# Performance work log

Measured on AMD Instinct MI355X. Metric: run time of the kernel, lower is better.

Reference implementation:

```python
import jax, jax.numpy as jnp
import numpy as np

B, N, D = 32, 2048, 1024


def setup_inputs() -> dict:
    key = jax.random.key(0)
    k1, k2, k3, k4, k5, k6 = jax.random.split(key, 6)
    encoded = jax.random.normal(k1, (B, N, D), dtype=jnp.float32)
    decoder_state = jax.random.normal(k2, (B, D), dtype=jnp.float32)
    mask = jax.random.randint(k3, (B, N), 0, 2, dtype=jnp.int32)
    scale = 1.0 / np.sqrt(D)
    W1 = jax.random.normal(k4, (D, D), dtype=jnp.float32) * scale  # applied as x @ W1
    W2 = jax.random.normal(k5, (D, D), dtype=jnp.float32) * scale
    vt = jax.random.normal(k6, (D,), dtype=jnp.float32) * scale
    return {"encoded": encoded, "decoder_state": decoder_state, "mask": mask,
            "W1": W1, "W2": W2, "vt": vt}


def reference(encoded, decoder_state, mask, W1, W2, vt):
    temperature = 1.0
    # process_encoded: W1(encoded)  [B, N, D]
    enc = jnp.einsum('bnd,de->bne', encoded, W1)
    # W2(decoder_state)  [B, D] -> broadcast-add over N
    dec = decoder_state @ W2
    # vt(tanh(.)).squeeze(2)  -> logits [B, N]
    u = jnp.einsum('bnd,d->bn', jnp.tanh(enc + dec[:, None, :]), vt)
    # masked log-softmax with temperature over dim=1
    logits = u / temperature + jnp.log(mask.astype(u.dtype) + 1e-45)
    return jax.nn.log_softmax(logits, axis=1)
```

## Files before the change

### kernel.cpp

```cpp
#include <hip/hip_runtime.h>

typedef _Float16 half8 __attribute__((ext_vector_type(8)));
typedef _Float16 half4 __attribute__((ext_vector_type(4)));
typedef __fp16   pk2   __attribute__((ext_vector_type(2)));
typedef float    f32x4 __attribute__((ext_vector_type(4)));

#define GLOBAL_AS __attribute__((address_space(1)))
#define LDS_AS    __attribute__((address_space(3)))

static constexpr int Bb = 32;
static constexpr int Nn = 2048;
static constexpr int Dd = 1024;
static constexpr int M  = Bb * Nn;


__global__ void prep0(const float* __restrict__ W1, _Float16* __restrict__ W1TT,
                      const float* __restrict__ ds, const float* __restrict__ W2,
                      float* __restrict__ dec) {
    const int id = blockIdx.x;
    const int tid = threadIdx.x;
    if (id < 512) {
        int g = id * 256 + tid;
        int chunk = g >> 10;
        int u = g & 1023;
        int q = u >> 7, sc = u & 127;
        int cl = sc ^ (2 * (q & 3));
        int et = chunk >> 5, t = (chunk >> 1) & 15, h = chunk & 1;
        int e  = et * 256 + h * 128 + cl;
        int k0 = t * 64 + q * 8;
        half8 hh;
#pragma unroll
        for (int j = 0; j < 8; ++j)
            hh[j] = (_Float16)W1[(size_t)(k0 + j) * Dd + e];
        *(half8*)(W1TT + (size_t)g * 8) = hh;
    } else {
        __shared__ float part[4][64];
        const int id2 = id - 512;
        const int b = id2 >> 4, ech = id2 & 15;
        int e = ech * 64 + (tid & 63);
        int dc = tid >> 6;
        float acc = 0.f;
#pragma unroll 4
        for (int d = dc * 256; d < dc * 256 + 256; ++d)
            acc += ds[b * Dd + d] * W2[(size_t)d * Dd + e];
        part[dc][tid & 63] = acc;
        __syncthreads();
        if (tid < 64)
            dec[b * Dd + e] = part[0][tid] + part[1][tid]
                            + part[2][tid] + part[3][tid];
    }
}

#define BAR     asm volatile("s_barrier" ::: "memory")
#define LGKM(n) asm volatile("s_waitcnt lgkmcnt(" #n ")" ::: "memory")
#define VM(n)   asm volatile("s_waitcnt vmcnt(" #n ")" ::: "memory")
#define PRIO1   __builtin_amdgcn_s_setprio(1)
#define PRIO0   __builtin_amdgcn_s_setprio(0)

#define RD_A(dst, base) do { _Pragma("unroll") \
  for (int ks = 0; ks < 2; ++ks) { \
    _Pragma("unroll") for (int m2 = 0; m2 < 4; ++m2) { \
      const int row_ = m2 * 32 + rA; \
      const int kc0_ = (ks * 4 + qq) * 2; \
      dst[m2][ks] = *(const half8*)&lds[(base) + (row_ * 16 + (kc0_ ^ rxa)) * 4]; \
    } } } while (0)

#define RD_B(dst, base) do { _Pragma("unroll") \
  for (int ks = 0; ks < 2; ++ks) { const int qb = ((ks * 4 + qq) * 128) * 8; \
    _Pragma("unroll") for (int j2 = 0; j2 < 2; ++j2) \
      dst[j2][ks] = *(const half8*)&lds[(base) + qb + (j2 * 64 + rB) * 8]; } } while (0)

#define MFMAQ(A_, B_, ro, co) do { \
  _Pragma("unroll") for (int m2 = 0; m2 < 4; ++m2) \
  _Pragma("unroll") for (int j2 = 0; j2 < 2; ++j2) { \
    acc[(ro) + m2][(co) + j2] = __builtin_amdgcn_mfma_f32_16x16x32_f16( \
        A_[m2][0], B_[j2][0], acc[(ro) + m2][(co) + j2], 0, 0, 0); \
    acc[(ro) + m2][(co) + j2] = __builtin_amdgcn_mfma_f32_16x16x32_f16( \
        A_[m2][1], B_[j2][1], acc[(ro) + m2][(co) + j2], 0, 0, 0); } } while (0)

__global__ __launch_bounds__(512, 2) void gemm8(
    const float* __restrict__ encA, const _Float16* __restrict__ W1TT,
    const float* __restrict__ dec, const float* __restrict__ vt,
    float* __restrict__ u_part)
{
    extern __shared__ _Float16 lds[];

    const int g  = blockIdx.x;
    const int wg = (g & 7) * 128 + (g >> 3);
    const int et    = wg & 3;
    const int mtile = wg >> 2;

    const int tid  = threadIdx.x;
    const int lane = tid & 63, wid = tid >> 6;
    const int wr = wid >> 2, wc = wid & 3;
    const int qq = lane >> 4, l15 = lane & 15;
    const int l15s = l15 ^ (2 * qq);
    const int rA = wr * 16 + l15;
    const int rxa = (l15 & 7) * 2;
    const int rB = wc * 16 + l15s;

    f32x4 acc[8][4] = {};
    half8 a[4][2], b0[2][2], b1[2][2];
    f32x4 aSt[8];

    const int arow0 = tid >> 4;
    const int l16   = tid & 15;
    const float* agp = encA + (((size_t)(mtile * 256 + arow0)) << 10) + l16 * 4;

    const size_t bbase = (size_t)et * 32 * 8192;
    const int uoff = tid * 8;

    auto issueA = [&](int T) {
        const float* gp = agp + T * 64;
#pragma unroll
        for (int p = 0; p < 8; ++p)
            aSt[p] = *(const f32x4*)(gp + ((size_t)p << 15));
    };
    auto writeA = [&](int Tn) {
        const int base = (Tn & 1) << 14;
#pragma unroll
        for (int p = 0; p < 8; ++p) {
            const int rf = p * 32 + arow0;
            const int h  = rf >> 7, row = rf & 127;
            pk2 c0 = __builtin_amdgcn_cvt_pkrtz(aSt[p][0], aSt[p][1]);
            pk2 c1 = __builtin_amdgcn_cvt_pkrtz(aSt[p][2], aSt[p][3]);
            half4 hh; hh[0] = c0[0]; hh[1] = c0[1]; hh[2] = c1[0]; hh[3] = c1[1];
            *(half4*)&lds[base + h * 8192
                          + (row * 16 + (l16 ^ ((row & 7) * 2))) * 4] = hh;
        }
    };
    auto stB = [&](int T, int h) {
        const _Float16* gp = W1TT + bbase + ((size_t)(T * 2 + h) << 13) + uoff;
        _Float16* lp = lds + (32768 + (((T & 1) * 2 + h) << 13) + (wid << 9));
        __builtin_amdgcn_global_load_lds((const GLOBAL_AS void*)gp,
                                         (LDS_AS void*)lp, 16, 0, 0);
        __builtin_amdgcn_global_load_lds((const GLOBAL_AS void*)(gp + 4096),
                                         (LDS_AS void*)(lp + 4096), 16, 0, 0);
    };


    issueA(0); stB(0, 0); stB(0, 1);
    VM(4);
    writeA(0);
    VM(0); LGKM(0);
    BAR;

#pragma unroll 2
    for (int T = 0; T < 16; ++T) {
        const int As  = (T & 1) << 14;
        const int Bs2 = 32768 + ((T & 1) << 14);
        const bool s = (T < 15);

        if (s) { issueA(T + 1); stB(T + 1, 0); stB(T + 1, 1); }

        RD_A(a, As);
        RD_B(b0, Bs2);
        RD_B(b1, Bs2 + 8192);
        LGKM(4);
        PRIO1; MFMAQ(a, b0, 0, 0); PRIO0;
        LGKM(0);
        PRIO1; MFMAQ(a, b1, 0, 2); PRIO0;
        RD_A(a, As + 8192);
        LGKM(0);
        PRIO1; MFMAQ(a, b0, 4, 0); MFMAQ(a, b1, 4, 2); PRIO0;

        if (s) { VM(4); writeA(T + 1); }
        VM(0); LGKM(0);
        BAR;
    }

    const int b = mtile >> 3;
    float vtv[4], dcv[4];
#pragma unroll
    for (int nf = 0; nf < 4; ++nf) {
        int e = et * 256 + (nf >> 1) * 128 + (nf & 1) * 64 + wc * 16 + l15;
        vtv[nf] = vt[e];
        dcv[nf] = dec[b * Dd + e];
    }
    float* usum = (float*)lds;
#pragma unroll
    for (int hm = 0; hm < 8; ++hm) {
        const int h = hm >> 2, mq = hm & 3;
#pragma unroll
        for (int r = 0; r < 4; ++r) {
            float sv = 0.f;
#pragma unroll
            for (int nf = 0; nf < 4; ++nf) {
                float x  = acc[hm][nf][r] + dcv[nf];
                float ex = __expf(2.f * x);
                sv += (1.f - 2.f * __builtin_amdgcn_rcpf(ex + 1.f)) * vtv[nf];
            }
#pragma unroll
            for (int off = 1; off < 16; off <<= 1) sv += __shfl_xor(sv, off, 16);
            if (l15 == 0)
                usum[wc * 256 + h * 128 + mq * 32 + wr * 16 + qq * 4 + r] = sv;
        }
    }
    __syncthreads();
    if (tid < 256) {
        float v = usum[tid] + usum[256 + tid] + usum[512 + tid] + usum[768 + tid];
        u_part[(size_t)et * M + (size_t)mtile * 256 + tid] = v;
    }
}

__global__ void softmax_k(const float* __restrict__ up, const int* __restrict__ mask,
                          float* __restrict__ out) {
    __shared__ float red[8];
    int b = blockIdx.x, tid = threadIdx.x;
    float l[8];
#pragma unroll
    for (int i = 0; i < 8; ++i) {
        int n = i * 256 + tid;
        float s = up[(size_t)b * Nn + n];
#pragma unroll
        for (int et = 1; et < 4; ++et) s += up[(size_t)et * M + (size_t)b * Nn + n];
        l[i] = s + (mask[b * Nn + n] ? 0.f : -103.278931f);
    }
    float m = l[0];
#pragma unroll
    for (int i = 1; i < 8; ++i) m = fmaxf(m, l[i]);
#pragma unroll
    for (int o = 32; o >= 1; o >>= 1) m = fmaxf(m, __shfl_xor(m, o, 64));
    if ((tid & 63) == 0) red[tid >> 6] = m;
    __syncthreads();
    m = fmaxf(fmaxf(red[0], red[1]), fmaxf(red[2], red[3]));
    float s = 0.f;
#pragma unroll
    for (int i = 0; i < 8; ++i) s += expf(l[i] - m);
#pragma unroll
    for (int o = 32; o >= 1; o >>= 1) s += __shfl_xor(s, o, 64);
    if ((tid & 63) == 0) red[4 + (tid >> 6)] = s;
    __syncthreads();
    float lse = m + logf(red[4] + red[5] + red[6] + red[7]);
#pragma unroll
    for (int i = 0; i < 8; ++i)
        out[(size_t)b * Nn + i * 256 + tid] = l[i] - lse;
}

extern "C" void kernel_launch(void* const* d_in, const int* in_sizes, int n_in,
                              void* d_out, int out_size, void* d_ws, size_t ws_size,
                              hipStream_t stream) {
    const float* encoded = (const float*)d_in[0];
    const float* dstate  = (const float*)d_in[1];
    const int*   mask    = (const int*)d_in[2];
    const float* W1      = (const float*)d_in[3];
    const float* W2      = (const float*)d_in[4];
    const float* vt      = (const float*)d_in[5];
    float* out = (float*)d_out;

    char* ws = (char*)d_ws;
    float*    u_part = (float*)ws;
    float*    dec    = (float*)(ws + (size_t)4 * M * 4);
    _Float16* W1TT   = (_Float16*)(ws + (size_t)4 * M * 4 + (size_t)Bb * Dd * 4);

    static bool attr_done = false;
    if (!attr_done) {
        hipFuncSetAttribute(reinterpret_cast<const void*>(gemm8),
                            hipFuncAttributeMaxDynamicSharedMemorySize, 131072);
        attr_done = true;
    }

    prep0<<<1024, 256, 0, stream>>>(W1, W1TT, dstate, W2, dec);
    gemm8<<<1024, 512, 131072, stream>>>(encoded, W1TT, dec, vt, u_part);
    softmax_k<<<32, 256, 0, stream>>>(u_part, mask, out);
}
```

Baseline: 525.1 us.

## Make each workgroup loop over all E-tiles for one M-tile

The grid shrinks from 1024 to 256 workgroups, and each one now walks all four output-column tiles for its row tile in one 64-step loop. The tanh/vt epilogue runs every 16 steps and the accumulators are reset. The aim is for the four re-reads of the same encoded rows to hit cache, and to avoid launch and tail overhead. In exchange it gives one workgroup per CU with less latency hiding, and needs extra LDS for the reduction buffer.

```diff
diff --git a/kernel.cpp b/kernel.cpp
--- a/kernel.cpp
+++ b/kernel.cpp
@@ -86,9 +86,7 @@
     extern __shared__ _Float16 lds[];
 
     const int g  = blockIdx.x;
-    const int wg = (g & 7) * 128 + (g >> 3);
-    const int et    = wg & 3;
-    const int mtile = wg >> 2;
+    const int mtile = (g & 7) * 32 + (g >> 3);
 
     const int tid  = threadIdx.x;
     const int lane = tid & 63, wid = tid >> 6;
@@ -107,11 +105,11 @@
     const int l16   = tid & 15;
     const float* agp = encA + (((size_t)(mtile * 256 + arow0)) << 10) + l16 * 4;
 
-    const size_t bbase = (size_t)et * 32 * 8192;
     const int uoff = tid * 8;
-
-    auto issueA = [&](int T) {
-        const float* gp = agp + T * 64;
+    float* usum = (float*)(lds + 65536);
+
+    auto issueA = [&](int Tn) {
+        const float* gp = agp + (Tn & 15) * 64;
 #pragma unroll
         for (int p = 0; p < 8; ++p)
             aSt[p] = *(const f32x4*)(gp + ((size_t)p << 15));
@@ -129,9 +127,9 @@
                           + (row * 16 + (l16 ^ ((row & 7) * 2))) * 4] = hh;
         }
     };
-    auto stB = [&](int T, int h) {
-        const _Float16* gp = W1TT + bbase + ((size_t)(T * 2 + h) << 13) + uoff;
-        _Float16* lp = lds + (32768 + (((T & 1) * 2 + h) << 13) + (wid << 9));
+    auto stB = [&](int Tn, int h) {
+        const _Float16* gp = W1TT + ((size_t)(Tn * 2 + h) << 13) + uoff;
+        _Float16* lp = lds + (32768 + (((Tn & 1) * 2 + h) << 13) + (wid << 9));
         __builtin_amdgcn_global_load_lds((const GLOBAL_AS void*)gp,
                                          (LDS_AS void*)lp, 16, 0, 0);
         __builtin_amdgcn_global_load_lds((const GLOBAL_AS void*)(gp + 4096),
@@ -146,12 +144,12 @@
     BAR;
 
 #pragma unroll 2
-    for (int T = 0; T < 16; ++T) {
-        const int As  = (T & 1) << 14;
-        const int Bs2 = 32768 + ((T & 1) << 14);
-        const bool s = (T < 15);
-
-        if (s) { issueA(T + 1); stB(T + 1, 0); stB(T + 1, 1); }
+    for (int t = 0; t < 64; ++t) {
+        const int As  = (t & 1) << 14;
+        const int Bs2 = 32768 + ((t & 1) << 14);
+        const bool s = (t < 63);
+
+        if (s) { issueA(t + 1); stB(t + 1, 0); stB(t + 1, 1); }
 
         RD_A(a, As);
         RD_B(b0, Bs2);
@@ -164,42 +162,52 @@
         LGKM(0);
         PRIO1; MFMAQ(a, b0, 4, 0); MFMAQ(a, b1, 4, 2); PRIO0;
 
-        if (s) { VM(4); writeA(T + 1); }
+        if (s) { VM(4); writeA(t + 1); }
         VM(0); LGKM(0);
         BAR;
-    }
-
-    const int b = mtile >> 3;
-    float vtv[4], dcv[4];
-#pragma unroll
-    for (int nf = 0; nf < 4; ++nf) {
-        int e = et * 256 + (nf >> 1) * 128 + (nf & 1) * 64 + wc * 16 + l15;
-        vtv[nf] = vt[e];
-        dcv[nf] = dec[b * Dd + e];
-    }
-    float* usum = (float*)lds;
-#pragma unroll
-    for (int hm = 0; hm < 8; ++hm) {
-        const int h = hm >> 2, mq = hm & 3;
-#pragma unroll
-        for (int r = 0; r < 4; ++r) {
-            float sv = 0.f;
+
+        if ((t & 15) == 15) {
+            const int et = t >> 4;
+            const int b = mtile >> 3;
+            float vtv[4], dcv[4];
 #pragma unroll
             for (int nf = 0; nf < 4; ++nf) {
-                float x  = acc[hm][nf][r] + dcv[nf];
-                float ex = __expf(2.f * x);
-                sv += (1.f - 2.f * __builtin_amdgcn_rcpf(ex + 1.f)) * vtv[nf];
+                int e = et * 256 + (nf >> 1) * 128 + (nf & 1) * 64 + wc * 16 + l15;
+                vtv[nf] = vt[e];
+                dcv[nf] = dec[b * Dd + e];
             }
-#pragma unroll
-            for (int off = 1; off < 16; off <<= 1) sv += __shfl_xor(sv, off, 16);
-            if (l15 == 0)
-                usum[wc * 256 + h * 128 + mq * 32 + wr * 16 + qq * 4 + r] = sv;
+            VM(0);
+#pragma unroll
+            for (int hm = 0; hm < 8; ++hm) {
+                const int h = hm >> 2, mq = hm & 3;
+#pragma unroll
+                for (int r = 0; r < 4; ++r) {
+                    float sv = 0.f;
+#pragma unroll
+                    for (int nf = 0; nf < 4; ++nf) {
+                        float x  = acc[hm][nf][r] + dcv[nf];
+                        float ex = __expf(2.f * x);
+                        sv += (1.f - 2.f * __builtin_amdgcn_rcpf(ex + 1.f)) * vtv[nf];
+                    }
+#pragma unroll
+                    for (int off = 1; off < 16; off <<= 1)
+                        sv += __shfl_xor(sv, off, 16);
+                    if (l15 == 0)
+                        usum[wc * 256 + h * 128 + mq * 32 + wr * 16 + qq * 4 + r] = sv;
+                }
+            }
+            LGKM(0); BAR;
+            if (tid < 256) {
+                float v = usum[tid] + usum[256 + tid]
+                        + usum[512 + tid] + usum[768 + tid];
+                u_part[(size_t)et * M + (size_t)mtile * 256 + tid] = v;
+            }
+#pragma unroll
+            for (int hm = 0; hm < 8; ++hm)
+#pragma unroll
+                for (int nf = 0; nf < 4; ++nf)
+                    acc[hm][nf] = (f32x4){0.f, 0.f, 0.f, 0.f};
         }
-    }
-    __syncthreads();
-    if (tid < 256) {
-        float v = usum[tid] + usum[256 + tid] + usum[512 + tid] + usum[768 + tid];
-        u_part[(size_t)et * M + (size_t)mtile * 256 + tid] = v;
     }
 }
 
@@ -256,11 +264,11 @@
     static bool attr_done = false;
     if (!attr_done) {
         hipFuncSetAttribute(reinterpret_cast<const void*>(gemm8),
-                            hipFuncAttributeMaxDynamicSharedMemorySize, 131072);
+                            hipFuncAttributeMaxDynamicSharedMemorySize, 135168);
         attr_done = true;
     }
 
     prep0<<<1024, 256, 0, stream>>>(W1, W1TT, dstate, W2, dec);
-    gemm8<<<1024, 512, 131072, stream>>>(encoded, W1TT, dec, vt, u_part);
+    gemm8<<<256, 512, 135168, stream>>>(encoded, W1TT, dec, vt, u_part);
     softmax_k<<<32, 256, 0, stream>>>(u_part, mask, out);
 }
```

Result: slower. 611.3 us (+16.4%).
